# Performance work log

Measured on AMD Instinct MI355X. Metric: run time of the kernel, lower is better.

Reference implementation:

```python
import jax, jax.numpy as jnp
import numpy as np

B, P, G = 64, 512, 64      # batch of independent nets, populations, generator inputs
N = P + G                   # presynaptic channels per population
H = 32                      # neuron-MLP hidden width
DT = 0.1                    # integration step (ms)
EREV_MIN, EREV_MAX = -75.0, 0.0


def setup_inputs() -> dict:
    key = jax.random.key(0)
    ks = jax.random.split(key, 16)
    state = jax.random.uniform(ks[0], (B, P), dtype=jnp.float32)          # prev firing rates
    inp = jax.random.uniform(ks[1], (B, G), dtype=jnp.float32)            # generator rates
    R = jnp.ones((B, P, N), dtype=jnp.float32)                            # recovered resources
    U = jnp.zeros((B, P, N), dtype=jnp.float32)                           # utilization
    A = jnp.zeros((B, P, N), dtype=jnp.float32)                           # active resources
    gsyn_max = 2.0 * jax.random.uniform(ks[2], (P, N), dtype=jnp.float32)
    pconn = jax.random.uniform(ks[3], (P, N), dtype=jnp.float32)
    Uinc = 0.1 + 0.5 * jax.random.uniform(ks[4], (P, N), dtype=jnp.float32)
    tau_r = 100.0 + 400.0 * jax.random.uniform(ks[5], (P, N), dtype=jnp.float32)  # recovery (ms)
    tau_f = 10.0 + 50.0 * jax.random.uniform(ks[6], (P, N), dtype=jnp.float32)    # facilitation
    tau_d = 2.0 + 5.0 * jax.random.uniform(ks[7], (P, N), dtype=jnp.float32)      # decay
    Erev = jnp.where(jax.random.uniform(ks[8], (P, N)) > 0.5, 0.0, -75.0).astype(jnp.float32)
    mask = jnp.ones((P, N), dtype=bool)                                   # is_connected_mask
    Cm = 0.5 + 2.0 * jax.random.uniform(ks[9], (P,), dtype=jnp.float32)
    W1 = 0.5 * jax.random.normal(ks[10], (P, 2, H), dtype=jnp.float32)
    b1 = 0.5 * jax.random.normal(ks[11], (P, H), dtype=jnp.float32)
    W2 = 0.5 * jax.random.normal(ks[12], (P, H, 1), dtype=jnp.float32)
    b2 = 0.5 * jax.random.normal(ks[13], (P, 1), dtype=jnp.float32)
    return {"state": state, "inp": inp, "R": R, "U": U, "A": A,
            "gsyn_max": gsyn_max, "pconn": pconn, "Uinc": Uinc,
            "tau_r": tau_r, "tau_f": tau_f, "tau_d": tau_d,
            "Erev": Erev, "mask": mask, "Cm": Cm,
            "W1": W1, "b1": b1, "W2": W2, "b2": b2}


def reference(state, inp, R, U, A, gsyn_max, pconn, Uinc, tau_r, tau_f, tau_d,
              Erev, mask, Cm, W1, b1, W2, b2):
    # --- TimeStepLayer.call: concat prev state with generator input -> full presyn vector
    x = jnp.concatenate([state, inp], axis=-1)                  # [B, N]
    SR = x[:, None, :] * pconn                                  # [B, P, N] spike prob per conn

    # --- TsodycsMarkramSynapse one Euler step (all populations fused)
    e_d = jnp.exp(-DT / tau_d)
    e_r = jnp.exp(-DT / tau_r)
    e_f = jnp.exp(-DT / tau_f)
    tau1r = jnp.where(tau_d != tau_r, tau_d / (tau_d - tau_r), 1e-13)
    a_dec = A * e_d
    r_dec = 1.0 + (R - 1.0 + tau1r * U) * e_r - tau1r * U
    u_dec = U * e_f
    u0 = u_dec + Uinc * (1.0 - u_dec) * SR                      # new utilization
    a0 = a_dec + u0 * r_dec * SR                                # new active fraction

    # --- synaptic drive features per population
    g = gsyn_max * a0 * mask                                    # [B, P, N]
    g_tot = jnp.sum(g, axis=-1)                                 # [B, P]
    E_eff = jnp.sum(g * Erev, axis=-1) / (g_tot + 1e-8)
    E_norm = (E_eff - EREV_MIN) / (EREV_MAX - EREV_MIN)
    g_norm = g_tot / (g_tot + Cm[None, :])
    feat = jnp.stack([E_norm, g_norm], axis=-1)                 # [B, P, 2]

    # --- frozen per-population neuron net (square activation, sigmoid rate)
    h = jnp.square(jnp.einsum('bpf,pfh->bph', feat, W1) + b1)   # [B, P, H]
    out = jax.nn.sigmoid(jnp.einsum('bph,pho->bpo', h, W2) + b2)[..., 0]  # [B, P]
    return out
```

## Files before the change

### kernel.cpp

```cpp
#include <hip/hip_runtime.h>

#define PP 512
#define GG 64
#define NN 576

#define PA(a, ch) lds_par[(a) * NN + (ch)]

#define DERIVE1(PC, UI, TR, TF, TD, GS, ER, Dpcg, Dup, Def, Der, Dc1, Dged, DEv) \
  {                                                                          \
    float e_r  = __expf(-0.1f * __builtin_amdgcn_rcpf(TR));                  \
    float e_f  = __expf(-0.1f * __builtin_amdgcn_rcpf(TF));                  \
    float e_d  = __expf(-0.1f * __builtin_amdgcn_rcpf(TD));                  \
    float diff = (TD) - (TR);                                                \
    float t1r  = (diff != 0.0f) ? (TD) * __builtin_amdgcn_rcpf(diff)         \
                                : 1e-13f;                                    \
    Dpcg = (PC) * (GS);                                                      \
    Dup  = (UI) * (PC);                                                      \
    Def  = e_f;                                                              \
    Der  = e_r;                                                              \
    Dc1  = t1r * (e_r - 1.0f);                                               \
    Dged = (GS) * e_d;                                                       \
    DEv  = (ER);                                                             \
  }

#define STEPQ(Vpcg, Vup, Vef, Ver, Vc1, Vged, VEv, Rv, Uv, Av, Xv)           \
  {                                                                          \
    float srg  = (Xv) * (Vpcg);                                              \
    float udec = (Uv) * (Vef);                                               \
    float upx  = (Vup) * (Xv);                                               \
    float u0   = udec + upx * (1.0f - udec);                                 \
    float rdec = 1.0f + ((Rv) - 1.0f) * (Ver) + (Vc1) * (Uv);                \
    float cg   = fmaf((Vged), (Av), srg * u0 * rdec);                        \
    gt += cg;                                                                \
    ge = fmaf((VEv), cg, ge);                                                \
  }

#define CHUNK(c, RV, UV, AV, XV)                                             \
  {                                                                          \
    const int ch = (c) * 256 + 4 * lane;                                     \
    float4 Qpcg = *(const float4*)&PA(0, ch);                                \
    float4 Qup  = *(const float4*)&PA(1, ch);                                \
    float4 Qef  = *(const float4*)&PA(2, ch);                                \
    float4 Qer  = *(const float4*)&PA(3, ch);                                \
    float4 Qc1  = *(const float4*)&PA(4, ch);                                \
    float4 Qged = *(const float4*)&PA(5, ch);                                \
    float4 QEv  = *(const float4*)&PA(6, ch);                                \
    STEPQ(Qpcg.x, Qup.x, Qef.x, Qer.x, Qc1.x, Qged.x, QEv.x,                 \
          (RV).x, (UV).x, (AV).x, (XV).x)                                    \
    STEPQ(Qpcg.y, Qup.y, Qef.y, Qer.y, Qc1.y, Qged.y, QEv.y,                 \
          (RV).y, (UV).y, (AV).y, (XV).y)                                    \
    STEPQ(Qpcg.z, Qup.z, Qef.z, Qer.z, Qc1.z, Qged.z, QEv.z,                 \
          (RV).z, (UV).z, (AV).z, (XV).z)                                    \
    STEPQ(Qpcg.w, Qup.w, Qef.w, Qer.w, Qc1.w, Qged.w, QEv.w,                 \
          (RV).w, (UV).w, (AV).w, (XV).w)                                    \
  }

__global__ __launch_bounds__(256, 4)
void timestep_kernel(const float* __restrict__ state,
                     const float* __restrict__ inp,
                     const float* __restrict__ R,
                     const float* __restrict__ U,
                     const float* __restrict__ A,
                     const float* __restrict__ gsyn_max,
                     const float* __restrict__ pconn,
                     const float* __restrict__ Uinc,
                     const float* __restrict__ tau_r,
                     const float* __restrict__ tau_f,
                     const float* __restrict__ tau_d,
                     const float* __restrict__ Erev,
                     const float* __restrict__ Cm,
                     const float* __restrict__ W1,
                     const float* __restrict__ b1,
                     const float* __restrict__ W2,
                     const float* __restrict__ b2,
                     float* __restrict__ out)
{
    __shared__ float lds_par[7 * NN];

    const int tid  = threadIdx.x;
    const int lane = tid & 63;
    const int wave = tid >> 6;
    const int p    = blockIdx.x >> 2;
    const int qtr  = blockIdx.x & 3;

    if (wave == 0) {
        const int prow = p * NN;
        #pragma unroll
        for (int c = 0; c < 2; ++c) {
            const int f4 = (prow >> 2) + c * 64 + lane;
            float4 v_pc = ((const float4*)pconn)[f4];
            float4 v_ui = ((const float4*)Uinc)[f4];
            float4 v_tr = ((const float4*)tau_r)[f4];
            float4 v_tf = ((const float4*)tau_f)[f4];
            float4 v_td = ((const float4*)tau_d)[f4];
            float4 v_gs = ((const float4*)gsyn_max)[f4];
            float4 v_er = ((const float4*)Erev)[f4];
            float4 Dpcg, Dup, Def, Der, Dc1, Dged, DEv;
            DERIVE1(v_pc.x, v_ui.x, v_tr.x, v_tf.x, v_td.x, v_gs.x, v_er.x,
                    Dpcg.x, Dup.x, Def.x, Der.x, Dc1.x, Dged.x, DEv.x)
            DERIVE1(v_pc.y, v_ui.y, v_tr.y, v_tf.y, v_td.y, v_gs.y, v_er.y,
                    Dpcg.y, Dup.y, Def.y, Der.y, Dc1.y, Dged.y, DEv.y)
            DERIVE1(v_pc.z, v_ui.z, v_tr.z, v_tf.z, v_td.z, v_gs.z, v_er.z,
                    Dpcg.z, Dup.z, Def.z, Der.z, Dc1.z, Dged.z, DEv.z)
            DERIVE1(v_pc.w, v_ui.w, v_tr.w, v_tf.w, v_td.w, v_gs.w, v_er.w,
                    Dpcg.w, Dup.w, Def.w, Der.w, Dc1.w, Dged.w, DEv.w)
            const int ch = c * 256 + 4 * lane;
            *(float4*)&PA(0, ch) = Dpcg;
            *(float4*)&PA(1, ch) = Dup;
            *(float4*)&PA(2, ch) = Def;
            *(float4*)&PA(3, ch) = Der;
            *(float4*)&PA(4, ch) = Dc1;
            *(float4*)&PA(5, ch) = Dged;
            *(float4*)&PA(6, ch) = DEv;
        }
        {
            const int o = prow + 512 + lane;
            float Dpcg, Dup, Def, Der, Dc1, Dged, DEv;
            DERIVE1(pconn[o], Uinc[o], tau_r[o], tau_f[o], tau_d[o],
                    gsyn_max[o], Erev[o],
                    Dpcg, Dup, Def, Der, Dc1, Dged, DEv)
            const int ch = 512 + lane;
            PA(0, ch) = Dpcg;  PA(1, ch) = Dup;  PA(2, ch) = Def;
            PA(3, ch) = Der;   PA(4, ch) = Dc1;  PA(5, ch) = Dged;
            PA(6, ch) = DEv;
        }
    }

    const int   j   = lane & 31;
    const float w1a = W1[p * 64 + j];
    const float w1b = W1[p * 64 + 32 + j];
    const float b1j = b1[p * 32 + j];
    const float w2j = W2[p * 32 + j];
    const float b2p = b2[p];
    const float cmp = Cm[p];

    __syncthreads();

    const int rot = (blockIdx.x >> 2) & 3;
    for (int t = 0; t < 4; ++t) {
        const int i = (t + rot) & 3;
        const int b = qtr * 16 + wave + 4 * i;

        const size_t rbase = ((size_t)b * PP + p) * (size_t)NN;
        const size_t r4    = rbase >> 2;
        const int    s4    = (b * PP) >> 2;

        float4 rv0 = ((const float4*)R)[r4 + lane];
        float4 uv0 = ((const float4*)U)[r4 + lane];
        float4 av0 = ((const float4*)A)[r4 + lane];
        float4 xv0 = ((const float4*)state)[s4 + lane];
        float4 rv1 = ((const float4*)R)[r4 + 64 + lane];
        float4 uv1 = ((const float4*)U)[r4 + 64 + lane];
        float4 av1 = ((const float4*)A)[r4 + 64 + lane];
        float4 xv1 = ((const float4*)state)[s4 + 64 + lane];
        const size_t o = rbase + 512 + (size_t)lane;
        float rts = R[o];
        float uts = U[o];
        float ats = A[o];
        float xts = inp[b * GG + lane];

        float gt = 0.0f, ge = 0.0f;
        CHUNK(0, rv0, uv0, av0, xv0)
        CHUNK(1, rv1, uv1, av1, xv1)
        {
            const int ch = 512 + lane;
            STEPQ(PA(0, ch), PA(1, ch), PA(2, ch), PA(3, ch), PA(4, ch),
                  PA(5, ch), PA(6, ch), rts, uts, ats, xts)
        }

        #pragma unroll
        for (int m = 32; m >= 1; m >>= 1) {
            gt += __shfl_xor(gt, m, 64);
            ge += __shfl_xor(ge, m, 64);
        }

        float Eeff = ge / (gt + 1e-8f);
        float En   = (Eeff + 75.0f) / 75.0f;
        float gn   = gt / (gt + cmp);
        float pre  = fmaf(En, w1a, fmaf(gn, w1b, b1j));
        float hv   = pre * pre;
        float v    = hv * w2j;
        #pragma unroll
        for (int m = 16; m >= 1; m >>= 1) v += __shfl_xor(v, m, 64);
        float s = v + b2p;
        float r = 1.0f / (1.0f + __expf(-s));
        if (lane == 0) out[(size_t)b * PP + p] = r;
    }
}

extern "C" void kernel_launch(void* const* d_in, const int* in_sizes, int n_in,
                              void* d_out, int out_size, void* d_ws, size_t ws_size,
                              hipStream_t stream) {
    const float* state = (const float*)d_in[0];
    const float* inp   = (const float*)d_in[1];
    const float* R     = (const float*)d_in[2];
    const float* U     = (const float*)d_in[3];
    const float* A     = (const float*)d_in[4];
    const float* gsyn  = (const float*)d_in[5];
    const float* pconn = (const float*)d_in[6];
    const float* Uinc  = (const float*)d_in[7];
    const float* taur  = (const float*)d_in[8];
    const float* tauf  = (const float*)d_in[9];
    const float* taud  = (const float*)d_in[10];
    const float* Erev  = (const float*)d_in[11];
    const float* Cm    = (const float*)d_in[13];
    const float* W1    = (const float*)d_in[14];
    const float* b1    = (const float*)d_in[15];
    const float* W2    = (const float*)d_in[16];
    const float* b2    = (const float*)d_in[17];
    float* out = (float*)d_out;

    hipLaunchKernelGGL(timestep_kernel, dim3(2048), dim3(256), 0, stream,
                       state, inp, R, U, A, gsyn, pconn, Uinc, taur, tauf, taud,
                       Erev, Cm, W1, b1, W2, b2, out);
}
```

Before: 258.7 us.

## Split parameter derivation into a pre-kernel and stream R/U/A over 4-population tiles

Adds a derive kernel that computes the per-synapse derived parameters once into the workspace and packs state/inp into a combined per-batch input row. The main kernel then processes 4 adjacent populations per block, so R/U/A reads are fully contiguous float4 loads across population boundaries, using split rounds and per-population accumulators. This spreads the transcendental parameter work across a whole grid instead of one wave per block, and cuts the grid to 512 blocks. The cost is an extra kernel launch and about 9.4 MB of extra workspace write/read traffic. A fallback to the old single kernel is kept for when the workspace is too small.

Result: slower. 300.0 us (+16.0%).

```diff
diff --git a/kernel.cpp b/kernel.cpp
--- a/kernel.cpp
+++ b/kernel.cpp
@@ -3,8 +3,11 @@
 #define PP 512
 #define GG 64
 #define NN 576
-
-#define PA(a, ch) lds_par[(a) * NN + (ch)]
+#define PN (PP * NN)
+#define PLANE4 (PN / 4)
+#define X4OFF (7 * PLANE4)
+#define XCHUNKS (64 * NN / 4)
+#define WS_BYTES ((size_t)(7 * PLANE4 + XCHUNKS) * 16)
 
 #define DERIVE1(PC, UI, TR, TF, TD, GS, ER, Dpcg, Dup, Def, Der, Dc1, Dged, DEv) \
   {                                                                          \
@@ -23,7 +26,192 @@
     DEv  = (ER);                                                             \
   }
 
-#define STEPQ(Vpcg, Vup, Vef, Ver, Vc1, Vged, VEv, Rv, Uv, Av, Xv)           \
+__global__ __launch_bounds__(256)
+void derive_kernel(const float* __restrict__ state,
+                   const float* __restrict__ inp,
+                   const float* __restrict__ gsyn_max,
+                   const float* __restrict__ pconn,
+                   const float* __restrict__ Uinc,
+                   const float* __restrict__ tau_r,
+                   const float* __restrict__ tau_f,
+                   const float* __restrict__ tau_d,
+                   const float* __restrict__ Erev,
+                   float4* __restrict__ ws4)
+{
+    const int cg = blockIdx.x * 256 + threadIdx.x;
+    float4 v_pc = ((const float4*)pconn)[cg];
+    float4 v_ui = ((const float4*)Uinc)[cg];
+    float4 v_tr = ((const float4*)tau_r)[cg];
+    float4 v_tf = ((const float4*)tau_f)[cg];
+    float4 v_td = ((const float4*)tau_d)[cg];
+    float4 v_gs = ((const float4*)gsyn_max)[cg];
+    float4 v_er = ((const float4*)Erev)[cg];
+    float4 Dpcg, Dup, Def, Der, Dc1, Dged, DEv;
+    DERIVE1(v_pc.x, v_ui.x, v_tr.x, v_tf.x, v_td.x, v_gs.x, v_er.x,
+            Dpcg.x, Dup.x, Def.x, Der.x, Dc1.x, Dged.x, DEv.x)
+    DERIVE1(v_pc.y, v_ui.y, v_tr.y, v_tf.y, v_td.y, v_gs.y, v_er.y,
+            Dpcg.y, Dup.y, Def.y, Der.y, Dc1.y, Dged.y, DEv.y)
+    DERIVE1(v_pc.z, v_ui.z, v_tr.z, v_tf.z, v_td.z, v_gs.z, v_er.z,
+            Dpcg.z, Dup.z, Def.z, Der.z, Dc1.z, Dged.z, DEv.z)
+    DERIVE1(v_pc.w, v_ui.w, v_tr.w, v_tf.w, v_td.w, v_gs.w, v_er.w,
+            Dpcg.w, Dup.w, Def.w, Der.w, Dc1.w, Dged.w, DEv.w)
+    ws4[0 * PLANE4 + cg] = Dpcg;
+    ws4[1 * PLANE4 + cg] = Dup;
+    ws4[2 * PLANE4 + cg] = Def;
+    ws4[3 * PLANE4 + cg] = Der;
+    ws4[4 * PLANE4 + cg] = Dc1;
+    ws4[5 * PLANE4 + cg] = Dged;
+    ws4[6 * PLANE4 + cg] = DEv;
+    if (cg < XCHUNKS) {
+        const int b = cg / 144, c = cg - b * 144;
+        float4 xv = (c < 128) ? ((const float4*)state)[b * 128 + c]
+                              : ((const float4*)inp)[b * 16 + (c - 128)];
+        ws4[X4OFF + cg] = xv;
+    }
+}
+
+
+#define E1(e)                                                                \
+  {                                                                          \
+    float srg  = xv.e * Qpcg.e;                                              \
+    float udec = uv.e * Qef.e;                                               \
+    float upx  = Qup.e * xv.e;                                               \
+    float u0   = udec + upx * (1.0f - udec);                                 \
+    float rdec = 1.0f + (rv.e - 1.0f) * Qer.e + Qc1.e * uv.e;                \
+    float cg   = fmaf(Qged.e, av.e, srg * u0 * rdec);                        \
+    sgt += cg;                                                               \
+    sge = fmaf(QEv.e, cg, sge);                                              \
+  }
+
+#define LOADS(i)                                                             \
+    const size_t q = cb + (size_t)(64 * (i)) + (size_t)lane;                 \
+    float4 rv = R4[q];                                                       \
+    float4 uv = U4[q];                                                       \
+    float4 av = A4[q];                                                       \
+    float4 Qpcg = ldsp[0 * 576 + 64 * (i) + lane];                           \
+    float4 Qup  = ldsp[1 * 576 + 64 * (i) + lane];                           \
+    float4 Qef  = ldsp[2 * 576 + 64 * (i) + lane];                           \
+    float4 Qer  = ldsp[3 * 576 + 64 * (i) + lane];                           \
+    float4 Qc1  = ldsp[4 * 576 + 64 * (i) + lane];                           \
+    float4 Qged = ldsp[5 * 576 + 64 * (i) + lane];                           \
+    float4 QEv  = ldsp[6 * 576 + 64 * (i) + lane];
+
+#define ROUND_FULL(i, K, OFF)                                                \
+  {                                                                          \
+    LOADS(i)                                                                 \
+    float4 xv = Xb[(OFF) + lane];                                            \
+    float sgt = 0.0f, sge = 0.0f;                                            \
+    E1(x) E1(y) E1(z) E1(w)                                                  \
+    gt##K += sgt;                                                            \
+    ge##K += sge;                                                            \
+  }
+
+#define ROUND_SPLIT(i, LB, K, KH, OFF)                                       \
+  {                                                                          \
+    LOADS(i)                                                                 \
+    const bool lo = lane < (LB);                                             \
+    const int  cm = lo ? ((OFF) + lane) : ((OFF) - 144 + lane);              \
+    float4 xv = Xb[cm];                                                      \
+    float sgt = 0.0f, sge = 0.0f;                                            \
+    E1(x) E1(y) E1(z) E1(w)                                                  \
+    gt##K  += lo ? sgt : 0.0f;                                               \
+    ge##K  += lo ? sge : 0.0f;                                               \
+    gt##KH += lo ? 0.0f : sgt;                                               \
+    ge##KH += lo ? 0.0f : sge;                                               \
+  }
+
+#define MLP_PAIR(GTL, GEL, GTH, GEH, W1A, W1B, B1, W2, B2, CM, FRB)          \
+  {                                                                          \
+    float gtv = hp ? (GTH) : (GTL);                                          \
+    float gev = hp ? (GEH) : (GEL);                                          \
+    float Eeff = gev / (gtv + 1e-8f);                                        \
+    float En   = (Eeff + 75.0f) / 75.0f;                                     \
+    float gn   = gtv / (gtv + (CM));                                         \
+    float pre  = fmaf(En, (W1A), fmaf(gn, (W1B), (B1)));                     \
+    float v    = pre * pre * (W2);                                           \
+    _Pragma("unroll")                                                        \
+    for (int m = 16; m >= 1; m >>= 1) v += __shfl_xor(v, m, 64);             \
+    float s = v + (B2);                                                      \
+    float r = 1.0f / (1.0f + __expf(-s));                                    \
+    if (lane == 0)  out[(FRB)]     = r;                                      \
+    if (lane == 32) out[(FRB) + 1] = r;                                      \
+  }
+
+__global__ __launch_bounds__(256, 2)
+void stream_kernel(const float* __restrict__ R,
+                   const float* __restrict__ U,
+                   const float* __restrict__ A,
+                   const float4* __restrict__ ws4,
+                   const float* __restrict__ Cm,
+                   const float* __restrict__ W1,
+                   const float* __restrict__ b1,
+                   const float* __restrict__ W2,
+                   const float* __restrict__ b2,
+                   float* __restrict__ out)
+{
+    __shared__ float4 ldsp[7 * 576];
+
+    const int tid  = threadIdx.x;
+    const int lane = tid & 63;
+    const int wave = tid >> 6;
+    const int pR   = (blockIdx.x & 127) * 4;
+    const int Wb   = blockIdx.x >> 7;
+
+    for (int idx = tid; idx < 7 * 576; idx += 256) {
+        const int a = idx / 576, c2 = idx - a * 576;
+        ldsp[idx] = ws4[a * PLANE4 + pR * 144 + c2];
+    }
+    __syncthreads();
+
+    const int j  = lane & 31;
+    const int hp = lane >> 5;
+    const int pA_ = pR + hp, pB_ = pR + 2 + hp;
+    const float w1aA = W1[pA_ * 64 + j], w1bA = W1[pA_ * 64 + 32 + j];
+    const float b1A = b1[pA_ * 32 + j], w2A = W2[pA_ * 32 + j];
+    const float b2A = b2[pA_], cmA = Cm[pA_];
+    const float w1aB = W1[pB_ * 64 + j], w1bB = W1[pB_ * 64 + 32 + j];
+    const float b1B = b1[pB_ * 32 + j], w2B = W2[pB_ * 32 + j];
+    const float b2B = b2[pB_], cmB = Cm[pB_];
+
+    const float4* R4 = (const float4*)R;
+    const float4* U4 = (const float4*)U;
+    const float4* A4 = (const float4*)A;
+
+    #pragma unroll 1
+    for (int t = 0; t < 4; ++t) {
+        const int b  = Wb * 16 + wave + 4 * t;
+        const int fr = b * PP + pR;
+        const size_t cb = (size_t)fr * 144;
+        const float4* Xb = ws4 + X4OFF + b * 144;
+
+        float gt0 = 0, gt1 = 0, gt2 = 0, gt3 = 0;
+        float ge0 = 0, ge1 = 0, ge2 = 0, ge3 = 0;
+
+        ROUND_FULL (0,        0, 0)
+        ROUND_FULL (1,        0, 64)
+        ROUND_SPLIT(2, 16, 0, 1, 128)
+        ROUND_FULL (3,        1, 48)
+        ROUND_SPLIT(4, 32, 1, 2, 112)
+        ROUND_FULL (5,        2, 32)
+        ROUND_SPLIT(6, 48, 2, 3, 96)
+        ROUND_FULL (7,        3, 16)
+        ROUND_FULL (8,        3, 80)
+
+        #pragma unroll
+        for (int m = 32; m >= 1; m >>= 1) {
+            gt0 += __shfl_xor(gt0, m, 64); ge0 += __shfl_xor(ge0, m, 64);
+            gt1 += __shfl_xor(gt1, m, 64); ge1 += __shfl_xor(ge1, m, 64);
+            gt2 += __shfl_xor(gt2, m, 64); ge2 += __shfl_xor(ge2, m, 64);
+            gt3 += __shfl_xor(gt3, m, 64); ge3 += __shfl_xor(ge3, m, 64);
+        }
+
+        MLP_PAIR(gt0, ge0, gt1, ge1, w1aA, w1bA, b1A, w2A, b2A, cmA, fr)
+        MLP_PAIR(gt2, ge2, gt3, ge3, w1aB, w1bB, b1B, w2B, b2B, cmB, fr + 2)
+    }
+}
+
+#define PA(a, ch) lds_par[(a) * NN + (ch)]
+#define STEPQ(Vpcg, Vup, Vef, Ver, Vc1, Vged, VEv, Rv, Uv, Av, Xv, GT, GE)   \
   {                                                                          \
     float srg  = (Xv) * (Vpcg);                                              \
     float udec = (Uv) * (Vef);                                               \
@@ -31,11 +219,10 @@
     float u0   = udec + upx * (1.0f - udec);                                 \
     float rdec = 1.0f + ((Rv) - 1.0f) * (Ver) + (Vc1) * (Uv);                \
     float cg   = fmaf((Vged), (Av), srg * u0 * rdec);                        \
-    gt += cg;                                                                \
-    ge = fmaf((VEv), cg, ge);                                                \
-  }
-
-#define CHUNK(c, RV, UV, AV, XV)                                             \
+    GT += cg;                                                                \
+    GE = fmaf((VEv), cg, GE);                                                \
+  }
+#define CHUNK1(c, RV, UV, AV, XV)                                            \
   {                                                                          \
     const int ch = (c) * 256 + 4 * lane;                                     \
     float4 Qpcg = *(const float4*)&PA(0, ch);                                \
@@ -46,43 +233,41 @@
     float4 Qged = *(const float4*)&PA(5, ch);                                \
     float4 QEv  = *(const float4*)&PA(6, ch);                                \
     STEPQ(Qpcg.x, Qup.x, Qef.x, Qer.x, Qc1.x, Qged.x, QEv.x,                 \
-          (RV).x, (UV).x, (AV).x, (XV).x)                                    \
+          (RV).x, (UV).x, (AV).x, (XV).x, gt0, ge0)                          \
     STEPQ(Qpcg.y, Qup.y, Qef.y, Qer.y, Qc1.y, Qged.y, QEv.y,                 \
-          (RV).y, (UV).y, (AV).y, (XV).y)                                    \
+          (RV).y, (UV).y, (AV).y, (XV).y, gt0, ge0)                          \
     STEPQ(Qpcg.z, Qup.z, Qef.z, Qer.z, Qc1.z, Qged.z, QEv.z,                 \
-          (RV).z, (UV).z, (AV).z, (XV).z)                                    \
+          (RV).z, (UV).z, (AV).z, (XV).z, gt0, ge0)                          \
     STEPQ(Qpcg.w, Qup.w, Qef.w, Qer.w, Qc1.w, Qged.w, QEv.w,                 \
-          (RV).w, (UV).w, (AV).w, (XV).w)                                    \
+          (RV).w, (UV).w, (AV).w, (XV).w, gt0, ge0)                          \
   }
 
 __global__ __launch_bounds__(256, 4)
-void timestep_kernel(const float* __restrict__ state,
-                     const float* __restrict__ inp,
-                     const float* __restrict__ R,
-                     const float* __restrict__ U,
-                     const float* __restrict__ A,
-                     const float* __restrict__ gsyn_max,
-                     const float* __restrict__ pconn,
-                     const float* __restrict__ Uinc,
-                     const float* __restrict__ tau_r,
-                     const float* __restrict__ tau_f,
-                     const float* __restrict__ tau_d,
-                     const float* __restrict__ Erev,
-                     const float* __restrict__ Cm,
-                     const float* __restrict__ W1,
-                     const float* __restrict__ b1,
-                     const float* __restrict__ W2,
-                     const float* __restrict__ b2,
-                     float* __restrict__ out)
+void timestep_fallback(const float* __restrict__ state,
+                       const float* __restrict__ inp,
+                       const float* __restrict__ R,
+                       const float* __restrict__ U,
+                       const float* __restrict__ A,
+                       const float* __restrict__ gsyn_max,
+                       const float* __restrict__ pconn,
+                       const float* __restrict__ Uinc,
+                       const float* __restrict__ tau_r,
+                       const float* __restrict__ tau_f,
+                       const float* __restrict__ tau_d,
+                       const float* __restrict__ Erev,
+                       const float* __restrict__ Cm,
+                       const float* __restrict__ W1,
+                       const float* __restrict__ b1,
+                       const float* __restrict__ W2,
+                       const float* __restrict__ b2,
+                       float* __restrict__ out)
 {
     __shared__ float lds_par[7 * NN];
-
     const int tid  = threadIdx.x;
     const int lane = tid & 63;
     const int wave = tid >> 6;
     const int p    = blockIdx.x >> 2;
     const int qtr  = blockIdx.x & 3;
-
     if (wave == 0) {
         const int prow = p * NN;
         #pragma unroll
@@ -114,7 +299,7 @@
             *(float4*)&PA(6, ch) = DEv;
         }
         {
-            const int o = prow + 512 + lane;
+            const int o = p * NN + 512 + lane;
             float Dpcg, Dup, Def, Der, Dc1, Dged, DEv;
             DERIVE1(pconn[o], Uinc[o], tau_r[o], tau_f[o], tau_d[o],
                     gsyn_max[o], Erev[o],
@@ -125,7 +310,6 @@
             PA(6, ch) = DEv;
         }
     }
-
     const int   j   = lane & 31;
     const float w1a = W1[p * 64 + j];
     const float w1b = W1[p * 64 + 32 + j];
@@ -133,18 +317,13 @@
     const float w2j = W2[p * 32 + j];
     const float b2p = b2[p];
     const float cmp = Cm[p];
-
     __syncthreads();
-
-    const int rot = (blockIdx.x >> 2) & 3;
+    #pragma unroll 1
     for (int t = 0; t < 4; ++t) {
-        const int i = (t + rot) & 3;
-        const int b = qtr * 16 + wave + 4 * i;
-
+        const int b = qtr * 16 + wave + 4 * t;
         const size_t rbase = ((size_t)b * PP + p) * (size_t)NN;
         const size_t r4    = rbase >> 2;
         const int    s4    = (b * PP) >> 2;
-
         float4 rv0 = ((const float4*)R)[r4 + lane];
         float4 uv0 = ((const float4*)U)[r4 + lane];
         float4 av0 = ((const float4*)A)[r4 + lane];
@@ -153,33 +332,28 @@
         float4 uv1 = ((const float4*)U)[r4 + 64 + lane];
         float4 av1 = ((const float4*)A)[r4 + 64 + lane];
         float4 xv1 = ((const float4*)state)[s4 + 64 + lane];
-        const size_t o = rbase + 512 + (size_t)lane;
-        float rts = R[o];
-        float uts = U[o];
-        float ats = A[o];
+        float rts = R[rbase + 512 + lane];
+        float uts = U[rbase + 512 + lane];
+        float ats = A[rbase + 512 + lane];
         float xts = inp[b * GG + lane];
-
-        float gt = 0.0f, ge = 0.0f;
-        CHUNK(0, rv0, uv0, av0, xv0)
-        CHUNK(1, rv1, uv1, av1, xv1)
+        float gt0 = 0.0f, ge0 = 0.0f;
+        CHUNK1(0, rv0, uv0, av0, xv0)
+        CHUNK1(1, rv1, uv1, av1, xv1)
         {
             const int ch = 512 + lane;
             STEPQ(PA(0, ch), PA(1, ch), PA(2, ch), PA(3, ch), PA(4, ch),
-                  PA(5, ch), PA(6, ch), rts, uts, ats, xts)
-        }
-
+                  PA(5, ch), PA(6, ch), rts, uts, ats, xts, gt0, ge0)
+        }
         #pragma unroll
         for (int m = 32; m >= 1; m >>= 1) {
-            gt += __shfl_xor(gt, m, 64);
-            ge += __shfl_xor(ge, m, 64);
-        }
-
-        float Eeff = ge / (gt + 1e-8f);
+            gt0 += __shfl_xor(gt0, m, 64);
+            ge0 += __shfl_xor(ge0, m, 64);
+        }
+        float Eeff = ge0 / (gt0 + 1e-8f);
         float En   = (Eeff + 75.0f) / 75.0f;
-        float gn   = gt / (gt + cmp);
+        float gn   = gt0 / (gt0 + cmp);
         float pre  = fmaf(En, w1a, fmaf(gn, w1b, b1j));
-        float hv   = pre * pre;
-        float v    = hv * w2j;
+        float v    = pre * pre * w2j;
         #pragma unroll
         for (int m = 16; m >= 1; m >>= 1) v += __shfl_xor(v, m, 64);
         float s = v + b2p;
@@ -210,7 +384,16 @@
     const float* b2    = (const float*)d_in[17];
     float* out = (float*)d_out;
 
-    hipLaunchKernelGGL(timestep_kernel, dim3(2048), dim3(256), 0, stream,
-                       state, inp, R, U, A, gsyn, pconn, Uinc, taur, tauf, taud,
-                       Erev, Cm, W1, b1, W2, b2, out);
+    if (ws_size >= WS_BYTES && d_ws != nullptr) {
+        float4* ws4 = (float4*)d_ws;
+        hipLaunchKernelGGL(derive_kernel, dim3(288), dim3(256), 0, stream,
+                           state, inp, gsyn, pconn, Uinc, taur, tauf, taud,
+                           Erev, ws4);
+        hipLaunchKernelGGL(stream_kernel, dim3(512), dim3(256), 0, stream,
+                           R, U, A, ws4, Cm, W1, b1, W2, b2, out);
+    } else {
+        hipLaunchKernelGGL(timestep_fallback, dim3(2048), dim3(256), 0, stream,
+                           state, inp, R, U, A, gsyn, pconn, Uinc, taur, tauf,
+                           taud, Erev, Cm, W1, b1, W2, b2, out);
+    }
 }
```
